# Kernel tuning notes

Measured on AMD Instinct MI355X. Metric: run time of the kernel, lower is better.

Reference implementation:

```python
import jax, jax.numpy as jnp
import numpy as np

N_NODES = 50000
N_EDGES = 600000
D = 128
LN_EPS = 1e-5


def _mlp_ln(x, W1, b1, W2, b2, g, beta):
    # Linear -> ReLU -> Linear -> LayerNorm (standard MeshGraphNets model_fn)
    h = jax.nn.relu(x @ W1 + b1)
    y = h @ W2 + b2
    mu = jnp.mean(y, axis=-1, keepdims=True)
    var = jnp.var(y, axis=-1, keepdims=True)
    return (y - mu) * jax.lax.rsqrt(var + LN_EPS) * g + beta


def setup_inputs() -> dict:
    key = jax.random.key(0)
    ks = jax.random.split(key, 16)
    def glorot(k, shape):
        fan = shape[0] + shape[1]
        return jax.random.normal(k, shape, jnp.float32) * np.sqrt(2.0 / fan)
    inp = {
        "node_features": jax.random.normal(ks[0], (1, N_NODES, D), jnp.float32),
        "edge_features": jax.random.normal(ks[1], (1, N_EDGES, D), jnp.float32),
        "senders": jax.random.randint(ks[2], (N_EDGES,), 0, N_NODES),
        "receivers": jax.random.randint(ks[3], (N_EDGES,), 0, N_NODES),
        # edge MLP: in 3*D -> 128 -> D, LayerNorm
        "eW1": glorot(ks[4], (3 * D, 128)), "eb1": jnp.zeros((128,), jnp.float32),
        "eW2": glorot(ks[5], (128, D)), "eb2": jnp.zeros((D,), jnp.float32),
        "eg": jnp.ones((D,), jnp.float32), "ebeta": jnp.zeros((D,), jnp.float32),
        # node MLP: in 2*D -> 128 -> D, LayerNorm
        "nW1": glorot(ks[6], (2 * D, 128)), "nb1": jnp.zeros((128,), jnp.float32),
        "nW2": glorot(ks[7], (128, D)), "nb2": jnp.zeros((D,), jnp.float32),
        "ng": jnp.ones((D,), jnp.float32), "nbeta": jnp.zeros((D,), jnp.float32),
        # attention linear D -> 1
        "aW": glorot(ks[8], (D, 1)), "ab": jnp.zeros((1,), jnp.float32),
    }
    return inp


def reference(node_features, edge_features, senders, receivers,
              eW1, eb1, eW2, eb2, eg, ebeta,
              nW1, nb1, nW2, nb2, ng, nbeta,
              aW, ab):
    # --- edge update: gather + concat + MLP ---
    sf = node_features[:, senders]      # [1,E,D]
    rf = node_features[:, receivers]    # [1,E,D]
    new_ef = _mlp_ln(jnp.concatenate([sf, rf, edge_features], -1),
                     eW1, eb1, eW2, eb2, eg, ebeta)  # [1,E,D]
    # --- per-edge attention: linear + LeakyReLU + scatter_softmax over receivers ---
    logits = jax.nn.leaky_relu(new_ef @ aW + ab, 0.2)[0, :, 0]  # [E]
    seg_max = jax.ops.segment_max(logits, receivers, num_segments=N_NODES)
    seg_max = jnp.where(jnp.isfinite(seg_max), seg_max, 0.0)
    ex = jnp.exp(logits - seg_max[receivers])
    seg_sum = jax.ops.segment_sum(ex, receivers, num_segments=N_NODES)
    att = ex / seg_sum[receivers]  # [E]
    # --- scatter-add aggregation ---
    agg = jax.ops.segment_sum(new_ef[0] * att[:, None], receivers,
                              num_segments=N_NODES)[None]  # [1,N,D]
    new_nf = _mlp_ln(jnp.concatenate([node_features, agg], -1),
                     nW1, nb1, nW2, nb2, ng, nbeta)  # [1,N,D]
    # residual connections
    new_nf = new_nf + node_features
    new_ef = new_ef + edge_features
    return new_nf, new_ef
```

## Files before the change

### kernel.cpp

```cpp
#include <hip/hip_runtime.h>
#include <hip/hip_bf16.h>

#define N_NODES 50000
#define N_EDGES 600000
#define D 128
#define LN_EPS 1e-5f

typedef float f32x4 __attribute__((ext_vector_type(4)));
typedef int   i32x4 __attribute__((ext_vector_type(4)));
typedef short s16x8 __attribute__((ext_vector_type(8)));

#define W1P_OFF     0u
#define W2P_OFF     98304u
#define NW1P_OFF    131072u
#define NW2P_OFF    196608u
#define DEG_OFF     229376u
#define ROWPTR_OFF  429440u
#define LOGITS_OFF  629504u
#define CURSOR_OFF  3029504u
#define ELIST_OFF   3229504u
#define AGG_OFF     5629504u
#define RAW_OFF     31229504u
#define WS_NEED_RAW (RAW_OFF + (size_t)N_EDGES * D * 2)

static __device__ __forceinline__ unsigned short f2bf(float f) {
    unsigned int u = __float_as_uint(f);
    u = (u + 0x7FFFu + ((u >> 16) & 1u)) >> 16;
    return (unsigned short)u;
}
static __device__ __forceinline__ float bf2f(unsigned short h) {
    return __uint_as_float(((unsigned int)h) << 16);
}
static __device__ __forceinline__ int pkbf2(float a, float b) {
    union { __hip_bfloat16 h[2]; int i; } u;
    u.h[0] = __float2bfloat16(a);
    u.h[1] = __float2bfloat16(b);
    return u.i;
}
union frag_u { i32x4 i; s16x8 s; };
static __device__ __forceinline__ f32x4 mfma_bf16(s16x8 a, s16x8 b, f32x4 c) {
    return __builtin_amdgcn_mfma_f32_16x16x32_bf16(a, b, c, 0, 0, 0);
}

__global__ void k_init(const float* __restrict__ eW1, const float* __restrict__ eW2,
                       const float* __restrict__ nW1, const float* __restrict__ nW2,
                       char* __restrict__ ws) {
    int idx = blockIdx.x * 256 + threadIdx.x;
    if (idx < N_NODES) {
        ((int*)(ws + DEG_OFF))[idx] = 0;
        ((int*)(ws + CURSOR_OFF))[idx] = 0;
    }
    int e = idx & 7, lane = (idx >> 3) & 63, ct = (idx >> 9) & 7, ks = idx >> 12;
    int k = ks * 32 + (lane >> 4) * 8 + e;
    int j = ct * 16 + (lane & 15);
    if (idx < 12 * 4096) ((unsigned short*)(ws + W1P_OFF))[idx]  = f2bf(eW1[k * 128 + j]);
    if (idx < 4 * 4096)  ((unsigned short*)(ws + W2P_OFF))[idx]  = f2bf(eW2[k * 128 + j]);
    if (idx < 8 * 4096)  ((unsigned short*)(ws + NW1P_OFF))[idx] = f2bf(nW1[k * 128 + j]);
    if (idx < 4 * 4096)  ((unsigned short*)(ws + NW2P_OFF))[idx] = f2bf(nW2[k * 128 + j]);
}

__global__ void k_count(const int* __restrict__ rcv, int* __restrict__ deg) {
    int e = blockIdx.x * 256 + threadIdx.x;
    if (e < N_EDGES) atomicAdd(&deg[rcv[e]], 1);
}

__global__ void k_scan(const int* __restrict__ deg, int* __restrict__ rowptr) {
    __shared__ int part[256];
    const int tid = threadIdx.x;
    const int CH = (N_NODES + 255) / 256;
    const int base = tid * CH;
    int s = 0;
    for (int i = 0; i < CH; ++i) { int idx = base + i; if (idx < N_NODES) s += deg[idx]; }
    part[tid] = s;
    __syncthreads();
    if (tid == 0) {
        int run = 0;
        for (int j = 0; j < 256; ++j) { int t = part[j]; part[j] = run; run += t; }
        rowptr[N_NODES] = run;
    }
    __syncthreads();
    int run = part[tid];
    for (int i = 0; i < CH; ++i) {
        int idx = base + i;
        if (idx < N_NODES) { rowptr[idx] = run; run += deg[idx]; }
    }
}

__global__ void k_fill(const int* __restrict__ rcv, const int* __restrict__ rowptr,
                       int* __restrict__ cursor, int* __restrict__ elist) {
    int e = blockIdx.x * 256 + threadIdx.x;
    if (e >= N_EDGES) return;
    int r = rcv[e];
    int slot = atomicAdd(&cursor[r], 1);
    elist[rowptr[r] + slot] = e;
}

template <int STORE_RAW>
__global__ __launch_bounds__(256, 4) void k_edge(
    const float* __restrict__ nf, const float* __restrict__ ef,
    const int* __restrict__ snd, const int* __restrict__ rcv,
    const i32x4* __restrict__ B1, const i32x4* __restrict__ B2,
    const float* __restrict__ b1, const float* __restrict__ b2,
    const float* __restrict__ g, const float* __restrict__ beta,
    const float* __restrict__ aW, const float* __restrict__ ab,
    float* __restrict__ out_ef, float* __restrict__ logits,
    unsigned short* __restrict__ rawbuf)
{
    __shared__ __align__(16) char  hbuf[64 * 128 * 2];
    __shared__ __align__(16) i32x4 bstage[2][512];
    const int tid = threadIdx.x, lane = tid & 63, rt = tid >> 6;
    const int j0 = lane & 15, hi = lane >> 4;

    const long eA = (long)blockIdx.x * 64 + rt * 16 + j0;
    const int sA = snd[eA], rA = rcv[eA];
    const float* __restrict__ prowS = nf + (size_t)sA * D;
    const float* __restrict__ prowR = nf + (size_t)rA * D;
    const float* __restrict__ prowE = ef + (size_t)eA * D;

    bstage[0][tid]       = B1[tid];
    bstage[0][256 + tid] = B1[256 + tid];
    __syncthreads();

    f32x4 acc[8];
    #pragma unroll
    for (int ct = 0; ct < 8; ++ct) acc[ct] = (f32x4){0.f, 0.f, 0.f, 0.f};
    for (int s = 0; s < 12; ++s) {
        const int cur = s & 1, nxt = cur ^ 1;
        const i32x4* src = (s + 1 < 12) ? (B1 + (s + 1) * 512) : B2;
        i32x4 t0 = src[tid], t1 = src[256 + tid];
        bstage[nxt][tid]       = t0;
        bstage[nxt][256 + tid] = t1;
        const float* p = (s < 4 ? prowS : (s < 8 ? prowR : prowE)) + (s & 3) * 32 + hi * 8;
        float4 f0 = *(const float4*)p;
        float4 f1 = *(const float4*)(p + 4);
        frag_u a;
        a.i[0] = pkbf2(f0.x, f0.y); a.i[1] = pkbf2(f0.z, f0.w);
        a.i[2] = pkbf2(f1.x, f1.y); a.i[3] = pkbf2(f1.z, f1.w);
        #pragma unroll
        for (int ct = 0; ct < 8; ++ct) {
            frag_u b; b.i = bstage[cur][ct * 64 + lane];
            acc[ct] = mfma_bf16(a.s, b.s, acc[ct]);
        }
        __syncthreads();
    }

    #pragma unroll
    for (int ct = 0; ct < 8; ++ct) {
        float bb = b1[ct * 16 + j0];
        #pragma unroll
        for (int rg = 0; rg < 4; ++rg) {
            int row = rt * 16 + hi * 4 + rg;
            float y = fmaxf(acc[ct][rg] + bb, 0.0f);
            int addr = (row * 256 + (ct * 16 + j0) * 2) ^ ((row & 7) << 4);
            *(__hip_bfloat16*)(hbuf + addr) = __float2bfloat16(y);
        }
    }
    asm volatile("" ::: "memory");

    #pragma unroll
    for (int ct = 0; ct < 8; ++ct) acc[ct] = (f32x4){0.f, 0.f, 0.f, 0.f};
    {
        const int arow = rt * 16 + j0;
        for (int s2 = 0; s2 < 4; ++s2) {
            const int cur = (12 + s2) & 1, nxt = cur ^ 1;
            if (s2 < 3) {
                const i32x4* src = B2 + (s2 + 1) * 512;
                i32x4 t0 = src[tid], t1 = src[256 + tid];
                bstage[nxt][tid]       = t0;
                bstage[nxt][256 + tid] = t1;
            }
            int addr = (arow * 256 + (s2 * 32 + hi * 8) * 2) ^ ((arow & 7) << 4);
            frag_u a;
            a.i = *(const i32x4*)(hbuf + addr);
            #pragma unroll
            for (int ct = 0; ct < 8; ++ct) {
                frag_u b; b.i = bstage[cur][ct * 64 + lane];
                acc[ct] = mfma_bf16(a.s, b.s, acc[ct]);
            }
            if (s2 < 3) __syncthreads();
        }
    }

    float b2v[8], gv[8], bv[8], awv[8];
    #pragma unroll
    for (int ct = 0; ct < 8; ++ct) {
        int c = ct * 16 + j0;
        b2v[ct] = b2[c]; gv[ct] = g[c]; bv[ct] = beta[c]; awv[ct] = aW[c];
    }
    float abv = ab[0];
    #pragma unroll
    for (int rg = 0; rg < 4; ++rg) {
        int row = rt * 16 + hi * 4 + rg;
        long e = (long)blockIdx.x * 64 + row;
        float y[8]; float s = 0.f, sq = 0.f;
        #pragma unroll
        for (int ct = 0; ct < 8; ++ct) {
            y[ct] = acc[ct][rg] + b2v[ct];
            s += y[ct]; sq += y[ct] * y[ct];
        }
        #pragma unroll
        for (int m = 1; m <= 8; m <<= 1) { s += __shfl_xor(s, m); sq += __shfl_xor(sq, m); }
        float mu = s * (1.0f / 128.0f);
        float var = sq * (1.0f / 128.0f) - mu * mu;
        float rs = rsqrtf(var + LN_EPS);
        const float* efr = ef + (size_t)e * D;
        float* outr = out_ef + (size_t)e * D;
        unsigned short* rawr = STORE_RAW ? (rawbuf + (size_t)e * D) : nullptr;
        float lg = 0.f;
        #pragma unroll
        for (int ct = 0; ct < 8; ++ct) {
            int c = ct * 16 + j0;
            float o = (y[ct] - mu) * rs * gv[ct] + bv[ct];
            outr[c] = o + efr[c];
            if (STORE_RAW) rawr[c] = f2bf(o);
            lg += o * awv[ct];
        }
        #pragma unroll
        for (int m = 1; m <= 8; m <<= 1) lg += __shfl_xor(lg, m);
        if (j0 == 0) {
            float L = lg + abv;
            L = (L >= 0.f) ? L : 0.2f * L;
            logits[e] = L;
        }
    }
}

template <int USE_RAW>
__global__ __launch_bounds__(256) void k_agg(
    const int* __restrict__ rowptr, const int* __restrict__ elist,
    const float* __restrict__ logits, const unsigned int* __restrict__ raw32,
    const float* __restrict__ out_ef, const float* __restrict__ ef,
    float* __restrict__ agg)
{
    const int tid = threadIdx.x, lane = tid & 63, w = tid >> 6;
    const int r = blockIdx.x * 4 + w;
    const int beg = rowptr[r], end = rowptr[r + 1];

    float mx = -3.4e38f;
    for (int cb = beg; cb < end; cb += 64) {
        int i = cb + lane;
        float lg = (i < end) ? logits[elist[i]] : -3.4e38f;
        mx = fmaxf(mx, lg);
    }
    #pragma unroll
    for (int m = 1; m <= 32; m <<= 1) mx = fmaxf(mx, __shfl_xor(mx, m));

    float ssum = 0.f, ax = 0.f, ay = 0.f;
    for (int cb = beg; cb < end; cb += 64) {
        int i = cb + lane;
        int cnt = min(64, end - cb);
        int e = (i < end) ? elist[i] : 0;
        float wt = (i < end) ? __expf(logits[e] - mx) : 0.f;
        ssum += wt;
        for (int j = 0; j < cnt; ++j) {
            int   ej = __shfl(e, j);
            float wj = __shfl(wt, j);
            if (USE_RAW) {
                unsigned int u = raw32[(size_t)ej * 64 + lane];
                ax += bf2f((unsigned short)(u & 0xffffu)) * wj;
                ay += bf2f((unsigned short)(u >> 16)) * wj;
            } else {
                float2 o = ((const float2*)out_ef)[(size_t)ej * 64 + lane];
                float2 f = ((const float2*)ef)[(size_t)ej * 64 + lane];
                ax += (o.x - f.x) * wj;
                ay += (o.y - f.y) * wj;
            }
        }
    }
    #pragma unroll
    for (int m = 1; m <= 32; m <<= 1) ssum += __shfl_xor(ssum, m);
    float inv = (ssum > 0.f) ? 1.0f / ssum : 0.0f;
    ((float2*)agg)[(size_t)r * 64 + lane] = make_float2(ax * inv, ay * inv);
}

__global__ __launch_bounds__(256, 4) void k_node(
    const float* __restrict__ nf, const float* __restrict__ agg,
    const s16x8* __restrict__ B1, const s16x8* __restrict__ B2,
    const float* __restrict__ b1, const float* __restrict__ b2,
    const float* __restrict__ g, const float* __restrict__ beta,
    float* __restrict__ out_nf)
{
    __shared__ __align__(16) char hbuf[64 * 128 * 2];
    const int tid = threadIdx.x, lane = tid & 63, rt = tid >> 6;
    const int j0 = lane & 15, hi = lane >> 4;

    long nA = (long)blockIdx.x * 64 + rt * 16 + j0;
    if (nA >= N_NODES) nA = 0;
    const float* __restrict__ prowN = nf  + (size_t)nA * D;
    const float* __restrict__ prowA = agg + (size_t)nA * D;

    f32x4 acc[8];
    #pragma unroll
    for (int ct = 0; ct < 8; ++ct) acc[ct] = (f32x4){0.f, 0.f, 0.f, 0.f};
    #pragma unroll
    for (int ks = 0; ks < 8; ++ks) {
        const float* p = (ks < 4 ? prowN : prowA) + (ks & 3) * 32 + hi * 8;
        float4 f0 = *(const float4*)p;
        float4 f1 = *(const float4*)(p + 4);
        frag_u a;
        a.i[0] = pkbf2(f0.x, f0.y); a.i[1] = pkbf2(f0.z, f0.w);
        a.i[2] = pkbf2(f1.x, f1.y); a.i[3] = pkbf2(f1.z, f1.w);
        #pragma unroll
        for (int ct = 0; ct < 8; ++ct)
            acc[ct] = mfma_bf16(a.s, B1[(ks * 8 + ct) * 64 + lane], acc[ct]);
    }

    #pragma unroll
    for (int ct = 0; ct < 8; ++ct) {
        float bb = b1[ct * 16 + j0];
        #pragma unroll
        for (int rg = 0; rg < 4; ++rg) {
            int row = rt * 16 + hi * 4 + rg;
            float y = fmaxf(acc[ct][rg] + bb, 0.0f);
            int addr = (row * 256 + (ct * 16 + j0) * 2) ^ ((row & 7) << 4);
            *(__hip_bfloat16*)(hbuf + addr) = __float2bfloat16(y);
        }
    }
    asm volatile("" ::: "memory");

    #pragma unroll
    for (int ct = 0; ct < 8; ++ct) acc[ct] = (f32x4){0.f, 0.f, 0.f, 0.f};
    {
        int arow = rt * 16 + j0;
        #pragma unroll
        for (int ks = 0; ks < 4; ++ks) {
            int addr = (arow * 256 + (ks * 32 + hi * 8) * 2) ^ ((arow & 7) << 4);
            frag_u a;
            a.i = *(const i32x4*)(hbuf + addr);
            #pragma unroll
            for (int ct = 0; ct < 8; ++ct)
                acc[ct] = mfma_bf16(a.s, B2[(ks * 8 + ct) * 64 + lane], acc[ct]);
        }
    }

    float b2v[8], gv[8], bv[8];
    #pragma unroll
    for (int ct = 0; ct < 8; ++ct) {
        int c = ct * 16 + j0;
        b2v[ct] = b2[c]; gv[ct] = g[c]; bv[ct] = beta[c];
    }
    #pragma unroll
    for (int rg = 0; rg < 4; ++rg) {
        int row = rt * 16 + hi * 4 + rg;
        long n = (long)blockIdx.x * 64 + row;
        float y[8]; float s = 0.f, sq = 0.f;
        #pragma unroll
        for (int ct = 0; ct < 8; ++ct) {
            y[ct] = acc[ct][rg] + b2v[ct];
            s += y[ct]; sq += y[ct] * y[ct];
        }
        #pragma unroll
        for (int m = 1; m <= 8; m <<= 1) { s += __shfl_xor(s, m); sq += __shfl_xor(sq, m); }
        float mu = s * (1.0f / 128.0f);
        float var = sq * (1.0f / 128.0f) - mu * mu;
        float rs = rsqrtf(var + LN_EPS);
        if (n < N_NODES) {
            const float* nfr = nf + (size_t)n * D;
            float* outr = out_nf + (size_t)n * D;
            #pragma unroll
            for (int ct = 0; ct < 8; ++ct) {
                int c = ct * 16 + j0;
                float o = (y[ct] - mu) * rs * gv[ct] + bv[ct];
                outr[c] = o + nfr[c];
            }
        }
    }
}

extern "C" void kernel_launch(void* const* d_in, const int* in_sizes, int n_in,
                              void* d_out, int out_size, void* d_ws, size_t ws_size,
                              hipStream_t stream)
{
    (void)in_sizes; (void)n_in; (void)out_size;
    const float* nf    = (const float*)d_in[0];
    const float* ef    = (const float*)d_in[1];
    const int*   snd   = (const int*)d_in[2];
    const int*   rcv   = (const int*)d_in[3];
    const float* eW1   = (const float*)d_in[4];
    const float* eb1   = (const float*)d_in[5];
    const float* eW2   = (const float*)d_in[6];
    const float* eb2   = (const float*)d_in[7];
    const float* eg    = (const float*)d_in[8];
    const float* ebeta = (const float*)d_in[9];
    const float* nW1   = (const float*)d_in[10];
    const float* nb1   = (const float*)d_in[11];
    const float* nW2   = (const float*)d_in[12];
    const float* nb2   = (const float*)d_in[13];
    const float* ng    = (const float*)d_in[14];
    const float* nbeta = (const float*)d_in[15];
    const float* aW    = (const float*)d_in[16];
    const float* ab    = (const float*)d_in[17];

    float* out_nf = (float*)d_out;
    float* out_ef = out_nf + (size_t)N_NODES * D;
    char*  ws     = (char*)d_ws;

    const bool use_raw = (ws_size >= WS_NEED_RAW);

    k_init<<<196, 256, 0, stream>>>(eW1, eW2, nW1, nW2, ws);

    k_count<<<(N_EDGES + 255) / 256, 256, 0, stream>>>(rcv, (int*)(ws + DEG_OFF));
    k_scan<<<1, 256, 0, stream>>>((const int*)(ws + DEG_OFF), (int*)(ws + ROWPTR_OFF));
    k_fill<<<(N_EDGES + 255) / 256, 256, 0, stream>>>(
        rcv, (const int*)(ws + ROWPTR_OFF), (int*)(ws + CURSOR_OFF), (int*)(ws + ELIST_OFF));

    if (use_raw) {
        k_edge<1><<<N_EDGES / 64, 256, 0, stream>>>(
            nf, ef, snd, rcv,
            (const i32x4*)(ws + W1P_OFF), (const i32x4*)(ws + W2P_OFF),
            eb1, eb2, eg, ebeta, aW, ab,
            out_ef, (float*)(ws + LOGITS_OFF), (unsigned short*)(ws + RAW_OFF));
        k_agg<1><<<N_NODES / 4, 256, 0, stream>>>(
            (const int*)(ws + ROWPTR_OFF), (const int*)(ws + ELIST_OFF),
            (const float*)(ws + LOGITS_OFF), (const unsigned int*)(ws + RAW_OFF),
            nullptr, nullptr, (float*)(ws + AGG_OFF));
    } else {
        k_edge<0><<<N_EDGES / 64, 256, 0, stream>>>(
            nf, ef, snd, rcv,
            (const i32x4*)(ws + W1P_OFF), (const i32x4*)(ws + W2P_OFF),
            eb1, eb2, eg, ebeta, aW, ab,
            out_ef, (float*)(ws + LOGITS_OFF), nullptr);
        k_agg<0><<<N_NODES / 4, 256, 0, stream>>>(
            (const int*)(ws + ROWPTR_OFF), (const int*)(ws + ELIST_OFF),
            (const float*)(ws + LOGITS_OFF), nullptr,
            out_ef, ef, (float*)(ws + AGG_OFF));
    }

    k_node<<<(N_NODES + 63) / 64, 256, 0, stream>>>(
        nf, (const float*)(ws + AGG_OFF),
        (const s16x8*)(ws + NW1P_OFF), (const s16x8*)(ws + NW2P_OFF),
        nb1, nb2, ng, nbeta, out_nf);
}
```

Baseline: 595.3 us.

## Make edge kernel persistent with both MLP weight matrices resident in LDS

The edge MLP kernel becomes persistent: 256 blocks of 512 threads grid-stride over 128-edge tiles. Each block loads both packed weight matrices (128KB) into LDS once. This removes the per-block, per-step double-buffered weight streaming and most of the barriers between K-steps. All 12 gathered input fragments are issued as loads up front to overlap gather latency. The cost is a 160KB LDS footprint, which allows only one block (8 waves) per CU, plus higher register pressure and some tail imbalance across tiles.

```diff
diff --git a/kernel.cpp b/kernel.cpp
--- a/kernel.cpp
+++ b/kernel.cpp
@@ -5,6 +5,7 @@
 #define N_EDGES 600000
 #define D 128
 #define LN_EPS 1e-5f
+#define NTILES ((N_EDGES + 127) / 128)
 
 typedef float f32x4 __attribute__((ext_vector_type(4)));
 typedef int   i32x4 __attribute__((ext_vector_type(4)));
@@ -96,90 +97,25 @@
 }
 
 template <int STORE_RAW>
-__global__ __launch_bounds__(256, 4) void k_edge(
+__global__ __launch_bounds__(512, 2) void k_edge(
     const float* __restrict__ nf, const float* __restrict__ ef,
     const int* __restrict__ snd, const int* __restrict__ rcv,
-    const i32x4* __restrict__ B1, const i32x4* __restrict__ B2,
+    const i32x4* __restrict__ Bg,
     const float* __restrict__ b1, const float* __restrict__ b2,
     const float* __restrict__ g, const float* __restrict__ beta,
     const float* __restrict__ aW, const float* __restrict__ ab,
     float* __restrict__ out_ef, float* __restrict__ logits,
     unsigned short* __restrict__ rawbuf)
 {
-    __shared__ __align__(16) char  hbuf[64 * 128 * 2];
-    __shared__ __align__(16) i32x4 bstage[2][512];
-    const int tid = threadIdx.x, lane = tid & 63, rt = tid >> 6;
+    __shared__ __align__(16) char lds[163840];
+    i32x4* Bl = (i32x4*)lds;
+    char* hbase = lds + 131072;
+    const int tid = threadIdx.x, lane = tid & 63, w = tid >> 6;
     const int j0 = lane & 15, hi = lane >> 4;
 
-    const long eA = (long)blockIdx.x * 64 + rt * 16 + j0;
-    const int sA = snd[eA], rA = rcv[eA];
-    const float* __restrict__ prowS = nf + (size_t)sA * D;
-    const float* __restrict__ prowR = nf + (size_t)rA * D;
-    const float* __restrict__ prowE = ef + (size_t)eA * D;
-
-    bstage[0][tid]       = B1[tid];
-    bstage[0][256 + tid] = B1[256 + tid];
+    #pragma unroll
+    for (int i = 0; i < 16; ++i) Bl[i * 512 + tid] = Bg[i * 512 + tid];
     __syncthreads();
-
-    f32x4 acc[8];
-    #pragma unroll
-    for (int ct = 0; ct < 8; ++ct) acc[ct] = (f32x4){0.f, 0.f, 0.f, 0.f};
-    for (int s = 0; s < 12; ++s) {
-        const int cur = s & 1, nxt = cur ^ 1;
-        const i32x4* src = (s + 1 < 12) ? (B1 + (s + 1) * 512) : B2;
-        i32x4 t0 = src[tid], t1 = src[256 + tid];
-        bstage[nxt][tid]       = t0;
-        bstage[nxt][256 + tid] = t1;
-        const float* p = (s < 4 ? prowS : (s < 8 ? prowR : prowE)) + (s & 3) * 32 + hi * 8;
-        float4 f0 = *(const float4*)p;
-        float4 f1 = *(const float4*)(p + 4);
-        frag_u a;
-        a.i[0] = pkbf2(f0.x, f0.y); a.i[1] = pkbf2(f0.z, f0.w);
-        a.i[2] = pkbf2(f1.x, f1.y); a.i[3] = pkbf2(f1.z, f1.w);
-        #pragma unroll
-        for (int ct = 0; ct < 8; ++ct) {
-            frag_u b; b.i = bstage[cur][ct * 64 + lane];
-            acc[ct] = mfma_bf16(a.s, b.s, acc[ct]);
-        }
-        __syncthreads();
-    }
-
-    #pragma unroll
-    for (int ct = 0; ct < 8; ++ct) {
-        float bb = b1[ct * 16 + j0];
-        #pragma unroll
-        for (int rg = 0; rg < 4; ++rg) {
-            int row = rt * 16 + hi * 4 + rg;
-            float y = fmaxf(acc[ct][rg] + bb, 0.0f);
-            int addr = (row * 256 + (ct * 16 + j0) * 2) ^ ((row & 7) << 4);
-            *(__hip_bfloat16*)(hbuf + addr) = __float2bfloat16(y);
-        }
-    }
-    asm volatile("" ::: "memory");
-
-    #pragma unroll
-    for (int ct = 0; ct < 8; ++ct) acc[ct] = (f32x4){0.f, 0.f, 0.f, 0.f};
-    {
-        const int arow = rt * 16 + j0;
-        for (int s2 = 0; s2 < 4; ++s2) {
-            const int cur = (12 + s2) & 1, nxt = cur ^ 1;
-            if (s2 < 3) {
-                const i32x4* src = B2 + (s2 + 1) * 512;
-                i32x4 t0 = src[tid], t1 = src[256 + tid];
-                bstage[nxt][tid]       = t0;
-                bstage[nxt][256 + tid] = t1;
-            }
-            int addr = (arow * 256 + (s2 * 32 + hi * 8) * 2) ^ ((arow & 7) << 4);
-            frag_u a;
-            a.i = *(const i32x4*)(hbuf + addr);
-            #pragma unroll
-            for (int ct = 0; ct < 8; ++ct) {
-                frag_u b; b.i = bstage[cur][ct * 64 + lane];
-                acc[ct] = mfma_bf16(a.s, b.s, acc[ct]);
-            }
-            if (s2 < 3) __syncthreads();
-        }
-    }
 
     float b2v[8], gv[8], bv[8], awv[8];
     #pragma unroll
@@ -187,40 +123,108 @@
         int c = ct * 16 + j0;
         b2v[ct] = b2[c]; gv[ct] = g[c]; bv[ct] = beta[c]; awv[ct] = aW[c];
     }
-    float abv = ab[0];
-    #pragma unroll
-    for (int rg = 0; rg < 4; ++rg) {
-        int row = rt * 16 + hi * 4 + rg;
-        long e = (long)blockIdx.x * 64 + row;
-        float y[8]; float s = 0.f, sq = 0.f;
+    const float abv = ab[0];
+    const float bb1[8] = { b1[0*16+j0], b1[1*16+j0], b1[2*16+j0], b1[3*16+j0],
+                           b1[4*16+j0], b1[5*16+j0], b1[6*16+j0], b1[7*16+j0] };
+
+    for (int tile = blockIdx.x; tile < NTILES; tile += 256) {
+        const long ebase = (long)tile * 128;
+        const long eA = ebase + w * 16 + j0;
+        const long eAc = (eA < N_EDGES) ? eA : (N_EDGES - 1);
+        const int sA = snd[eAc], rA = rcv[eAc];
+        const float* __restrict__ pS = nf + (size_t)sA * D;
+        const float* __restrict__ pR = nf + (size_t)rA * D;
+        const float* __restrict__ pE = ef + (size_t)eAc * D;
+
+        float4 fa0[12], fa1[12];
+        #pragma unroll
+        for (int s = 0; s < 12; ++s) {
+            const float* p = (s < 4 ? pS : (s < 8 ? pR : pE)) + (s & 3) * 32 + hi * 8;
+            fa0[s] = *(const float4*)p;
+            fa1[s] = *(const float4*)(p + 4);
+        }
+
+        f32x4 acc[8];
+        #pragma unroll
+        for (int ct = 0; ct < 8; ++ct) acc[ct] = (f32x4){0.f, 0.f, 0.f, 0.f};
+        #pragma unroll
+        for (int s = 0; s < 12; ++s) {
+            frag_u a;
+            a.i[0] = pkbf2(fa0[s].x, fa0[s].y); a.i[1] = pkbf2(fa0[s].z, fa0[s].w);
+            a.i[2] = pkbf2(fa1[s].x, fa1[s].y); a.i[3] = pkbf2(fa1[s].z, fa1[s].w);
+            #pragma unroll
+            for (int ct = 0; ct < 8; ++ct) {
+                frag_u b; b.i = Bl[(s * 8 + ct) * 64 + lane];
+                acc[ct] = mfma_bf16(a.s, b.s, acc[ct]);
+            }
+        }
+
         #pragma unroll
         for (int ct = 0; ct < 8; ++ct) {
-            y[ct] = acc[ct][rg] + b2v[ct];
-            s += y[ct]; sq += y[ct] * y[ct];
-        }
-        #pragma unroll
-        for (int m = 1; m <= 8; m <<= 1) { s += __shfl_xor(s, m); sq += __shfl_xor(sq, m); }
-        float mu = s * (1.0f / 128.0f);
-        float var = sq * (1.0f / 128.0f) - mu * mu;
-        float rs = rsqrtf(var + LN_EPS);
-        const float* efr = ef + (size_t)e * D;
-        float* outr = out_ef + (size_t)e * D;
-        unsigned short* rawr = STORE_RAW ? (rawbuf + (size_t)e * D) : nullptr;
-        float lg = 0.f;
-        #pragma unroll
-        for (int ct = 0; ct < 8; ++ct) {
-            int c = ct * 16 + j0;
-            float o = (y[ct] - mu) * rs * gv[ct] + bv[ct];
-            outr[c] = o + efr[c];
-            if (STORE_RAW) rawr[c] = f2bf(o);
-            lg += o * awv[ct];
-        }
-        #pragma unroll
-        for (int m = 1; m <= 8; m <<= 1) lg += __shfl_xor(lg, m);
-        if (j0 == 0) {
-            float L = lg + abv;
-            L = (L >= 0.f) ? L : 0.2f * L;
-            logits[e] = L;
+            #pragma unroll
+            for (int rg = 0; rg < 4; ++rg) {
+                int row = w * 16 + hi * 4 + rg;
+                float y = fmaxf(acc[ct][rg] + bb1[ct], 0.0f);
+                int rel = (row * 256 + (ct * 16 + j0) * 2) ^ ((row & 7) << 4);
+                *(__hip_bfloat16*)(hbase + rel) = __float2bfloat16(y);
+            }
+        }
+        __syncthreads();
+
+        #pragma unroll
+        for (int ct = 0; ct < 8; ++ct) acc[ct] = (f32x4){0.f, 0.f, 0.f, 0.f};
+        {
+            const int arow = w * 16 + j0;
+            #pragma unroll
+            for (int s2 = 0; s2 < 4; ++s2) {
+                int rel = (arow * 256 + (s2 * 32 + hi * 8) * 2) ^ ((arow & 7) << 4);
+                frag_u a;
+                a.i = *(const i32x4*)(hbase + rel);
+                #pragma unroll
+                for (int ct = 0; ct < 8; ++ct) {
+                    frag_u b; b.i = Bl[6144 + (s2 * 8 + ct) * 64 + lane];
+                    acc[ct] = mfma_bf16(a.s, b.s, acc[ct]);
+                }
+            }
+        }
+        __syncthreads();
+
+        #pragma unroll
+        for (int rg = 0; rg < 4; ++rg) {
+            int row = w * 16 + hi * 4 + rg;
+            long e = ebase + row;
+            float y[8]; float s = 0.f, sq = 0.f;
+            #pragma unroll
+            for (int ct = 0; ct < 8; ++ct) {
+                y[ct] = acc[ct][rg] + b2v[ct];
+                s += y[ct]; sq += y[ct] * y[ct];
+            }
+            #pragma unroll
+            for (int m = 1; m <= 8; m <<= 1) { s += __shfl_xor(s, m); sq += __shfl_xor(sq, m); }
+            float mu = s * (1.0f / 128.0f);
+            float var = sq * (1.0f / 128.0f) - mu * mu;
+            float rs = rsqrtf(var + LN_EPS);
+            float lg = 0.f;
+            if (e < N_EDGES) {
+                const float* efr = ef + (size_t)e * D;
+                float* outr = out_ef + (size_t)e * D;
+                unsigned short* rawr = STORE_RAW ? (rawbuf + (size_t)e * D) : nullptr;
+                #pragma unroll
+                for (int ct = 0; ct < 8; ++ct) {
+                    int c = ct * 16 + j0;
+                    float o = (y[ct] - mu) * rs * gv[ct] + bv[ct];
+                    outr[c] = o + efr[c];
+                    if (STORE_RAW) rawr[c] = f2bf(o);
+                    lg += o * awv[ct];
+                }
+            }
+            #pragma unroll
+            for (int m = 1; m <= 8; m <<= 1) lg += __shfl_xor(lg, m);
+            if (j0 == 0 && e < N_EDGES) {
+                float L = lg + abv;
+                L = (L >= 0.f) ? L : 0.2f * L;
+                logits[e] = L;
+            }
         }
     }
 }
@@ -405,9 +409,8 @@
         rcv, (const int*)(ws + ROWPTR_OFF), (int*)(ws + CURSOR_OFF), (int*)(ws + ELIST_OFF));
 
     if (use_raw) {
-        k_edge<1><<<N_EDGES / 64, 256, 0, stream>>>(
-            nf, ef, snd, rcv,
-            (const i32x4*)(ws + W1P_OFF), (const i32x4*)(ws + W2P_OFF),
+        k_edge<1><<<256, 512, 0, stream>>>(
+            nf, ef, snd, rcv, (const i32x4*)(ws + W1P_OFF),
             eb1, eb2, eg, ebeta, aW, ab,
             out_ef, (float*)(ws + LOGITS_OFF), (unsigned short*)(ws + RAW_OFF));
         k_agg<1><<<N_NODES / 4, 256, 0, stream>>>(
@@ -415,9 +418,8 @@
             (const float*)(ws + LOGITS_OFF), (const unsigned int*)(ws + RAW_OFF),
             nullptr, nullptr, (float*)(ws + AGG_OFF));
     } else {
-        k_edge<0><<<N_EDGES / 64, 256, 0, stream>>>(
-            nf, ef, snd, rcv,
-            (const i32x4*)(ws + W1P_OFF), (const i32x4*)(ws + W2P_OFF),
+        k_edge<0><<<256, 512, 0, stream>>>(
+            nf, ef, snd, rcv, (const i32x4*)(ws + W1P_OFF),
             eb1, eb2, eg, ebeta, aW, ab,
             out_ef, (float*)(ws + LOGITS_OFF), nullptr);
         k_agg<0><<<N_NODES / 4, 256, 0, stream>>>(
```

After: 602.5 us. Within noise of the previous version (+1.2%).
